# Performance work log

Hardware: AMD Instinct MI355X
Metric: run time of the kernel (lower is better)

The kernel has to match this reference:

```python
import jax, jax.numpy as jnp
import numpy as np

N, C, E, S = 16384, 128, 262144, 10
AVG_NUM_NEIGHBORS = 16.0
INV_SQRT3 = 1.0 / np.sqrt(3.0)


def setup_inputs() -> dict:
    key = jax.random.key(0)
    ks = jax.random.split(key, 15)
    return dict(
        node_specie=jax.random.randint(ks[0], (N,), 0, S),
        node_feats=jax.random.normal(ks[1], (N, C, 4), jnp.float32),   # irreps 0e+1o per channel
        edge_attrs=jax.random.normal(ks[2], (E, 4), jnp.float32),      # Y: 0e+1o
        edge_feats=jax.random.normal(ks[3], (E, 8), jnp.float32),      # radial scalars
        senders=jax.random.randint(ks[4], (E,), 0, N),
        receivers=jax.random.randint(ks[5], (E,), 0, N),
        W_sc0=jax.random.normal(ks[6], (S, C, C), jnp.float32),
        W_sc1=jax.random.normal(ks[7], (S, C, C), jnp.float32),
        W_pre0=jax.random.normal(ks[8], (C, C), jnp.float32),
        W_pre1=jax.random.normal(ks[9], (C, C), jnp.float32),
        W_mlp1=jax.random.normal(ks[10], (8, 64), jnp.float32),
        W_mlp2=jax.random.normal(ks[11], (64, 64), jnp.float32),
        W_mlp3=jax.random.normal(ks[12], (64, 4), jnp.float32),
        W_post0=jax.random.normal(ks[13], (C, 2, C), jnp.float32),
        W_post1=jax.random.normal(ks[14], (C, 2, C), jnp.float32),
    )


def reference(node_specie, node_feats, edge_attrs, edge_feats, senders, receivers,
              W_sc0, W_sc1, W_pre0, W_pre1, W_mlp1, W_mlp2, W_mlp3, W_post0, W_post1):
    inv_c = 1.0 / np.sqrt(C)
    s_in = node_feats[..., 0]      # [N,C] 0e
    v_in = node_feats[..., 1:4]    # [N,C,3] 1o

    # linear_sc: per-species equivariant linear (0e+1o -> hidden 0e+1o)
    sc_s = jnp.einsum('nc,ncd->nd', s_in, W_sc0[node_specie]) * inv_c
    sc_v = jnp.einsum('nci,ncd->ndi', v_in, W_sc1[node_specie]) * inv_c
    sc = jnp.concatenate([sc_s[..., None], sc_v], axis=-1)  # [N,C,4]

    # linear_premp: channel-mixing equivariant linear (same irreps)
    s = (s_in @ W_pre0) * inv_c                              # [N,C]
    v = jnp.einsum('nci,cd->ndi', v_in, W_pre1) * inv_c      # [N,C,3]

    # MessagePassingConvolution (channel axis kept instead of hk.vmap)
    se_s = s[senders]              # [E,C]
    se_v = v[senders]              # [E,C,3]
    a = edge_attrs[:, 1:4]         # drop 0e part of Y -> 1o
    dot = jnp.einsum('eci,ei->ec', se_v, a) * INV_SQRT3      # 1o x 1o -> 0e
    sva = se_s[..., None] * a[:, None, :]                    # 0e x 1o -> 1o

    # radial MLP -> one mixing scalar per irrep (num_irreps = 4), shared across channels
    h = jax.nn.silu((edge_feats @ W_mlp1) * (1.0 / np.sqrt(8.0)))
    h = jax.nn.silu((h @ W_mlp2) * 0.125)
    mix = (h @ W_mlp3) * 0.125                               # [E,4]

    # messages irreps 2x0e+2x1o: [s, dot | v, s*a], each block scaled by its mix scalar
    msg = jnp.concatenate([
        se_s[..., None] * mix[:, None, 0:1],
        dot[..., None] * mix[:, None, 1:2],
        se_v * mix[:, None, 2:3],
        sva * mix[:, None, 3:4],
    ], axis=-1)                                              # [E,C,8]

    agg = jnp.zeros((N, C, 8), msg.dtype).at[receivers].add(msg) / AVG_NUM_NEIGHBORS

    # linear_postmp: (2x0e+2x1o, C channels) -> (0e+1o, C channels)
    inv2c = 1.0 / np.sqrt(2 * C)
    o_s = jnp.einsum('ncm,cmd->nd', agg[..., :2], W_post0) * inv2c
    o_v = jnp.einsum('ncmi,cmd->ndi', agg[..., 2:].reshape(N, C, 2, 3), W_post1) * inv2c
    node_out = jnp.concatenate([o_s[..., None], o_v], axis=-1)  # [N,C,4]
    return node_out, sc
```

## Files before the change

### kernel.cpp

```cpp
#include <hip/hip_runtime.h>
#include <hip/hip_bf16.h>

#define N_NODES 16384
#define C_DIM   128
#define E_EDGES 262144
#define S_SPEC  10
#define CHUNK   256
#define PROWS   16544
#define PTILES  1034

__device__ __constant__ const float INV_C  = 0.08838834764831845f;
__device__ __constant__ const float INV_2C = 0.0625f;
#define F_INV_SQRT3 0.5773502691896258f
#define F_INV_SQRT8 0.35355339059327373f
#define F_INV_AVG   0.0625f

typedef __attribute__((ext_vector_type(8))) short bf16x8;
typedef __attribute__((ext_vector_type(4))) float f32x4;

__device__ __forceinline__ float silu(float x) {
    return x / (1.0f + __expf(-x));
}

__device__ __forceinline__ unsigned short f2bf(float x) {
    __hip_bfloat16 h = __float2bfloat16(x);
    return *reinterpret_cast<unsigned short*>(&h);
}

__device__ __forceinline__ unsigned int pack2bf(float lo, float hi) {
    return (unsigned int)f2bf(lo) | ((unsigned int)f2bf(hi) << 16);
}

__device__ __forceinline__ float bf2f(unsigned int u16) {
    return __uint_as_float((u16 & 0xffffu) << 16);
}

__device__ __forceinline__ float bf2f_hi(unsigned int u) {
    return __uint_as_float(u & 0xffff0000u);
}

__global__ __launch_bounds__(256) void init_kernel(
    int* __restrict__ counts, int* __restrict__ scnt,
    int* __restrict__ prow_map, int* __restrict__ tile_spec)
{
    const int idx = blockIdx.x * 256 + threadIdx.x;
    if (idx < N_NODES) counts[idx] = 0;
    if (idx < S_SPEC)  scnt[idx] = 0;
    if (idx < PROWS)   prow_map[idx] = -1;
    if (idx < PTILES)  tile_spec[idx] = 0;
}

__global__ __launch_bounds__(256) void hist_kernel(
    const int* __restrict__ receivers, int* __restrict__ cnt,
    const int* __restrict__ specie, int* __restrict__ scnt)
{
    __shared__ int h[S_SPEC];
    const int t = threadIdx.x;
    const bool doSpec = blockIdx.x < (N_NODES / 256);
    if (doSpec) {
        if (t < S_SPEC) h[t] = 0;
        __syncthreads();
        atomicAdd(&h[specie[blockIdx.x * 256 + t]], 1);
    }
    const int e = blockIdx.x * 256 + t;
    atomicAdd(&cnt[receivers[e]], 1);
    if (doSpec) {
        __syncthreads();
        if (t < S_SPEC) atomicAdd(&scnt[t], h[t]);
    }
}

__global__ __launch_bounds__(256) void scan_kernel(
    const int* __restrict__ cnt, int* __restrict__ start,
    int* __restrict__ cursor,
    const int* __restrict__ scnt, int* __restrict__ poff,
    int* __restrict__ scur)
{
    __shared__ int sums[256];
    const int t = threadIdx.x;
    if (t == 0) {
        int pa = 0;
        for (int i = 0; i < S_SPEC; ++i) {
            poff[i] = pa;
            scur[i] = 0;
            pa += ((scnt[i] + 15) >> 4) << 4;
        }
    }
    int s = 0;
    for (int i = 0; i < 64; ++i) s += cnt[t * 64 + i];
    sums[t] = s;
    __syncthreads();
    if (t == 0) {
        int a = 0;
        for (int i = 0; i < 256; ++i) { int v = sums[i]; sums[i] = a; a += v; }
    }
    __syncthreads();
    int a = sums[t];
    for (int i = 0; i < 64; ++i) {
        int v = cnt[t * 64 + i];
        start[t * 64 + i] = a;
        cursor[t * 64 + i] = a;
        a += v;
    }
    if (t == 255) start[N_NODES] = a;
}

__global__ __launch_bounds__(256) void scatter_place_kernel(
    const int* __restrict__ receivers, int* __restrict__ cursor,
    int* __restrict__ perm,
    const int* __restrict__ specie, const int* __restrict__ poff,
    int* __restrict__ scur,
    int* __restrict__ prow_map, int* __restrict__ tile_spec)
{
    const int t = threadIdx.x;
    const int e = blockIdx.x * 256 + t;
    const int pos = atomicAdd(&cursor[receivers[e]], 1);
    perm[pos] = e;

    if (blockIdx.x < (N_NODES / 256)) {
        __shared__ int h[S_SPEC];
        __shared__ int bbase[S_SPEC];
        if (t < S_SPEC) h[t] = 0;
        __syncthreads();
        const int n = blockIdx.x * 256 + t;
        const int s = specie[n];
        const int lrank = atomicAdd(&h[s], 1);
        __syncthreads();
        if (t < S_SPEC && h[t] > 0) bbase[t] = atomicAdd(&scur[t], h[t]);
        __syncthreads();
        const int p = poff[s] + bbase[s] + lrank;
        prow_map[p] = n;
        tile_spec[p >> 4] = s;
    }
}

__global__ __launch_bounds__(256) void prep_kernel(
    const int* __restrict__ prow_map, const float* __restrict__ node_feats,
    ushort* __restrict__ As, ushort* __restrict__ Av0,
    ushort* __restrict__ Av1, ushort* __restrict__ Av2,
    const float* __restrict__ Wsc0, const float* __restrict__ Wsc1,
    ushort* __restrict__ Wsc0t, ushort* __restrict__ Wsc1t,
    const float* __restrict__ Wpre0, const float* __restrict__ Wpre1,
    ushort* __restrict__ Wpre0t, ushort* __restrict__ Wpre1t,
    const float* __restrict__ Wp0, const float* __restrict__ Wp1,
    ushort* __restrict__ Bt0, ushort* __restrict__ Bt1,
    const float* __restrict__ Wm1, const float* __restrict__ Wm2,
    const float* __restrict__ Wm3,
    ushort* __restrict__ W1t, ushort* __restrict__ W2t,
    ushort* __restrict__ W3t)
{
    const int idx = blockIdx.x * 256 + threadIdx.x;
    {
        const int p = idx >> 7, c = idx & 127;
        const int nid = prow_map[p];
        float4 f = {0.0f, 0.0f, 0.0f, 0.0f};
        if (nid >= 0) f = ((const float4*)node_feats)[nid * C_DIM + c];
        As [idx] = f2bf(f.x);
        Av0[idx] = f2bf(f.y);
        Av1[idx] = f2bf(f.z);
        Av2[idx] = f2bf(f.w);
    }
    if (idx < S_SPEC * 128 * 128) {
        const int s = idx >> 14, d = (idx >> 7) & 127, k = idx & 127;
        Wsc0t[idx] = f2bf(Wsc0[s * 16384 + k * 128 + d] * INV_C);
        Wsc1t[idx] = f2bf(Wsc1[s * 16384 + k * 128 + d] * INV_C);
    }
    if (idx < 16384) {
        const int d = idx >> 7, k = idx & 127;
        Wpre0t[idx] = f2bf(Wpre0[k * 128 + d] * INV_C);
        Wpre1t[idx] = f2bf(Wpre1[k * 128 + d] * INV_C);
    }
    if (idx < 32768) {
        const int k = idx >> 7, d = idx & 127;
        Bt0[d * 256 + k] = f2bf(Wp0[idx] * INV_2C);
        Bt1[d * 256 + k] = f2bf(Wp1[idx] * INV_2C);
    }
    if (idx < 4096) {
        if (idx < 2048) {
            const int hh = idx >> 5, k = idx & 31;
            W1t[idx] = (k < 8) ? f2bf(Wm1[k * 64 + hh] * F_INV_SQRT8) : (ushort)0;
        }
        {
            const int c = idx >> 6, k = idx & 63;
            W2t[idx] = f2bf(Wm2[k * 64 + c] * 0.125f);
        }
        if (idx < 1024) {
            const int m = idx >> 6, k = idx & 63;
            W3t[idx] = (m < 4) ? f2bf(Wm3[k * 4 + m] * 0.125f) : (ushort)0;
        }
    }
}

__global__ __launch_bounds__(512) void node_gemm_kernel(
    const int* __restrict__ prow_map,
    const int* __restrict__ tile_spec,
    const ushort* __restrict__ As,
    const ushort* __restrict__ Av0,
    const ushort* __restrict__ Av1,
    const ushort* __restrict__ Av2,
    const ushort* __restrict__ Wsc0t,
    const ushort* __restrict__ Wsc1t,
    const ushort* __restrict__ Wpre0t,
    const ushort* __restrict__ Wpre1t,
    float* __restrict__ out_sc,
    ushort4* __restrict__ sv_bf)
{
    const int l  = threadIdx.x & 63;
    const int w  = threadIdx.x >> 6;
    const int d0 = w * 16;
    const int lr = l & 15;
    const int lg = l >> 4;

    bf16x8 bp0[4], bp1[4];
#pragma unroll
    for (int ks = 0; ks < 4; ++ks) {
        bp0[ks] = *reinterpret_cast<const bf16x8*>(
            Wpre0t + (d0 + lr) * 128 + ks * 32 + lg * 8);
        bp1[ks] = *reinterpret_cast<const bf16x8*>(
            Wpre1t + (d0 + lr) * 128 + ks * 32 + lg * 8);
    }

    const int tile = blockIdx.x;
    const int sp   = tile_spec[tile];
    const int r0   = tile * 16;

    const ushort* as  = As  + (size_t)(r0 + lr) * 128 + lg * 8;
    const ushort* av0 = Av0 + (size_t)(r0 + lr) * 128 + lg * 8;
    const ushort* av1 = Av1 + (size_t)(r0 + lr) * 128 + lg * 8;
    const ushort* av2 = Av2 + (size_t)(r0 + lr) * 128 + lg * 8;
    const ushort* ws0 = Wsc0t + (size_t)sp * 16384 + (d0 + lr) * 128 + lg * 8;
    const ushort* ws1 = Wsc1t + (size_t)sp * 16384 + (d0 + lr) * 128 + lg * 8;

    const f32x4 zero = {0.0f, 0.0f, 0.0f, 0.0f};
    f32x4 aS0 = zero, aS1 = zero, aS2 = zero, aS3 = zero;
    f32x4 aP0 = zero, aP1 = zero, aP2 = zero, aP3 = zero;

#pragma unroll
    for (int ks = 0; ks < 4; ++ks) {
        const bf16x8 a_s  = *reinterpret_cast<const bf16x8*>(as  + ks * 32);
        const bf16x8 a_v0 = *reinterpret_cast<const bf16x8*>(av0 + ks * 32);
        const bf16x8 a_v1 = *reinterpret_cast<const bf16x8*>(av1 + ks * 32);
        const bf16x8 a_v2 = *reinterpret_cast<const bf16x8*>(av2 + ks * 32);
        const bf16x8 bs0  = *reinterpret_cast<const bf16x8*>(ws0 + ks * 32);
        const bf16x8 bs1  = *reinterpret_cast<const bf16x8*>(ws1 + ks * 32);
        aS0 = __builtin_amdgcn_mfma_f32_16x16x32_bf16(a_s,  bs0, aS0, 0, 0, 0);
        aS1 = __builtin_amdgcn_mfma_f32_16x16x32_bf16(a_v0, bs1, aS1, 0, 0, 0);
        aS2 = __builtin_amdgcn_mfma_f32_16x16x32_bf16(a_v1, bs1, aS2, 0, 0, 0);
        aS3 = __builtin_amdgcn_mfma_f32_16x16x32_bf16(a_v2, bs1, aS3, 0, 0, 0);
        aP0 = __builtin_amdgcn_mfma_f32_16x16x32_bf16(a_s,  bp0[ks], aP0, 0, 0, 0);
        aP1 = __builtin_amdgcn_mfma_f32_16x16x32_bf16(a_v0, bp1[ks], aP1, 0, 0, 0);
        aP2 = __builtin_amdgcn_mfma_f32_16x16x32_bf16(a_v1, bp1[ks], aP2, 0, 0, 0);
        aP3 = __builtin_amdgcn_mfma_f32_16x16x32_bf16(a_v2, bp1[ks], aP3, 0, 0, 0);
    }

#pragma unroll
    for (int r = 0; r < 4; ++r) {
        const int row = r0 + lg * 4 + r;
        const int nid = prow_map[row];
        if (nid >= 0) {
            float4 o = {aS0[r], aS1[r], aS2[r], aS3[r]};
            ((float4*)out_sc)[(size_t)nid * C_DIM + (d0 + lr)] = o;
            ushort4 pv = {f2bf(aP0[r]), f2bf(aP1[r]), f2bf(aP2[r]), f2bf(aP3[r])};
            sv_bf[(size_t)nid * C_DIM + (d0 + lr)] = pv;
        }
    }
}

__global__ __launch_bounds__(256) void edge_mlp_mfma_kernel(
    const float* __restrict__ edge_feats,
    const float* __restrict__ edge_attrs,
    const ushort* __restrict__ W1t,
    const ushort* __restrict__ W2t,
    const ushort* __restrict__ W3t,
    uint4* __restrict__ coefbf)
{
    __shared__ ushort h_lds[4][16][72];

    const int w  = threadIdx.x >> 6;
    const int l  = threadIdx.x & 63;
    const int lr = l & 15;
    const int lg = l >> 4;

    bf16x8 a1[4];
#pragma unroll
    for (int mt = 0; mt < 4; ++mt)
        a1[mt] = *reinterpret_cast<const bf16x8*>(
            W1t + (mt * 16 + lr) * 32 + lg * 8);
    bf16x8 a2[4][2];
#pragma unroll
    for (int mt = 0; mt < 4; ++mt)
#pragma unroll
        for (int ks = 0; ks < 2; ++ks)
            a2[mt][ks] = *reinterpret_cast<const bf16x8*>(
                W2t + (mt * 16 + lr) * 64 + ks * 32 + lg * 8);
    bf16x8 a3[2];
#pragma unroll
    for (int ks = 0; ks < 2; ++ks)
        a3[ks] = *reinterpret_cast<const bf16x8*>(
            W3t + lr * 64 + ks * 32 + lg * 8);

    const int tile = blockIdx.x * 4 + w;
    const int e0   = tile * 16;
    const f32x4 zero = {0.0f, 0.0f, 0.0f, 0.0f};

    bf16x8 b1 = {0, 0, 0, 0, 0, 0, 0, 0};
    if (lg == 0) {
        const float4 q0 = *(const float4*)(edge_feats + (size_t)(e0 + lr) * 8);
        const float4 q1 = *(const float4*)(edge_feats + (size_t)(e0 + lr) * 8 + 4);
        b1[0] = (short)f2bf(q0.x); b1[1] = (short)f2bf(q0.y);
        b1[2] = (short)f2bf(q0.z); b1[3] = (short)f2bf(q0.w);
        b1[4] = (short)f2bf(q1.x); b1[5] = (short)f2bf(q1.y);
        b1[6] = (short)f2bf(q1.z); b1[7] = (short)f2bf(q1.w);
    }

    f32x4 d1[4];
#pragma unroll
    for (int mt = 0; mt < 4; ++mt)
        d1[mt] = __builtin_amdgcn_mfma_f32_16x16x32_bf16(a1[mt], b1, zero, 0, 0, 0);

#pragma unroll
    for (int mt = 0; mt < 4; ++mt) {
        uint2 p;
        p.x = pack2bf(silu(d1[mt][0]), silu(d1[mt][1]));
        p.y = pack2bf(silu(d1[mt][2]), silu(d1[mt][3]));
        *reinterpret_cast<uint2*>(&h_lds[w][lr][mt * 16 + lg * 4]) = p;
    }
    __syncthreads();

    bf16x8 b2[2];
#pragma unroll
    for (int ks = 0; ks < 2; ++ks)
        b2[ks] = *reinterpret_cast<const bf16x8*>(
            &h_lds[w][lr][ks * 32 + lg * 8]);

    f32x4 d2[4];
#pragma unroll
    for (int mt = 0; mt < 4; ++mt) {
        d2[mt] = __builtin_amdgcn_mfma_f32_16x16x32_bf16(a2[mt][0], b2[0], zero, 0, 0, 0);
        d2[mt] = __builtin_amdgcn_mfma_f32_16x16x32_bf16(a2[mt][1], b2[1], d2[mt], 0, 0, 0);
    }

#pragma unroll
    for (int mt = 0; mt < 4; ++mt) {
        uint2 p;
        p.x = pack2bf(silu(d2[mt][0]), silu(d2[mt][1]));
        p.y = pack2bf(silu(d2[mt][2]), silu(d2[mt][3]));
        *reinterpret_cast<uint2*>(&h_lds[w][lr][mt * 16 + lg * 4]) = p;
    }
    __syncthreads();

    bf16x8 b3[2];
#pragma unroll
    for (int ks = 0; ks < 2; ++ks)
        b3[ks] = *reinterpret_cast<const bf16x8*>(
            &h_lds[w][lr][ks * 32 + lg * 8]);

    f32x4 d3;
    d3 = __builtin_amdgcn_mfma_f32_16x16x32_bf16(a3[0], b3[0], zero, 0, 0, 0);
    d3 = __builtin_amdgcn_mfma_f32_16x16x32_bf16(a3[1], b3[1], d3, 0, 0, 0);

    if (lg == 0) {
        const int e = e0 + lr;
        const float4 a = *(const float4*)(edge_attrs + (size_t)e * 4);
        const float mx0 = d3[0], mx1 = d3[1], mx2 = d3[2], mx3 = d3[3];
        uint4 cv;
        cv.x = pack2bf(mx0,                      mx1 * a.y * F_INV_SQRT3);
        cv.y = pack2bf(mx1 * a.z * F_INV_SQRT3,  mx1 * a.w * F_INV_SQRT3);
        cv.z = pack2bf(mx2,                      mx3 * a.y);
        cv.w = pack2bf(mx3 * a.z,                mx3 * a.w);
        coefbf[e] = cv;
    }
}

__global__ __launch_bounds__(256) void agg_kernel(
    const int* __restrict__ start,
    const int* __restrict__ perm,
    const int* __restrict__ senders,
    const uint4* __restrict__ coefbf,
    const ushort4* __restrict__ sv_bf,
    unsigned int* __restrict__ A_s,
    unsigned int* __restrict__ A_v)
{
    __shared__ int   se_lds[CHUNK];
    __shared__ float sc_lds[CHUNK][8];

    const int n0   = blockIdx.x * 8;
    const int t    = threadIdx.x;
    const int c    = t & 127;
    const int half = t >> 7;

    int nbeg[4], nend[4];
#pragma unroll
    for (int k = 0; k < 4; ++k) {
        nbeg[k] = start[n0 + half * 4 + k];
        nend[k] = start[n0 + half * 4 + k + 1];
    }

    const int blk_beg = start[n0];
    const int blk_end = start[n0 + 8];

    float acc[4][8] = {};

    for (int cb = blk_beg; cb < blk_end; cb += CHUNK) {
        const int cn = min(CHUNK, blk_end - cb);
        __syncthreads();
        for (int j = t; j < cn; j += 256) {
            const int e = perm[cb + j];
            se_lds[j] = senders[e];
            const uint4 cv = coefbf[e];
            float4 lo = {bf2f(cv.x), bf2f_hi(cv.x), bf2f(cv.y), bf2f_hi(cv.y)};
            float4 hi = {bf2f(cv.z), bf2f_hi(cv.z), bf2f(cv.w), bf2f_hi(cv.w)};
            ((float4*)sc_lds[j])[0] = lo;
            ((float4*)sc_lds[j])[1] = hi;
        }
        __syncthreads();

#pragma unroll
        for (int k = 0; k < 4; ++k) {
            const int lo = max(nbeg[k], cb);
            const int hi = min(nend[k], cb + cn);
            int idx = lo;
            for (; idx + 2 <= hi; idx += 2) {
                const int j0 = idx - cb, j1 = j0 + 1;
                const int snd0 = se_lds[j0];
                const int snd1 = se_lds[j1];
                const ushort4 u0 = sv_bf[(size_t)snd0 * C_DIM + c];
                const ushort4 u1 = sv_bf[(size_t)snd1 * C_DIM + c];
                const float* kf0 = sc_lds[j0];
                const float* kf1 = sc_lds[j1];
                const float x0 = bf2f(u0.x), y0 = bf2f(u0.y),
                            z0 = bf2f(u0.z), w0 = bf2f(u0.w);
                const float x1 = bf2f(u1.x), y1 = bf2f(u1.y),
                            z1 = bf2f(u1.z), w1 = bf2f(u1.w);
                acc[k][0] += x0 * kf0[0];
                acc[k][1] += y0 * kf0[1] + z0 * kf0[2] + w0 * kf0[3];
                acc[k][2] += y0 * kf0[4];
                acc[k][3] += z0 * kf0[4];
                acc[k][4] += w0 * kf0[4];
                acc[k][5] += x0 * kf0[5];
                acc[k][6] += x0 * kf0[6];
                acc[k][7] += x0 * kf0[7];
                acc[k][0] += x1 * kf1[0];
                acc[k][1] += y1 * kf1[1] + z1 * kf1[2] + w1 * kf1[3];
                acc[k][2] += y1 * kf1[4];
                acc[k][3] += z1 * kf1[4];
                acc[k][4] += w1 * kf1[4];
                acc[k][5] += x1 * kf1[5];
                acc[k][6] += x1 * kf1[6];
                acc[k][7] += x1 * kf1[7];
            }
            if (idx < hi) {
                const int j = idx - cb;
                const int snd = se_lds[j];
                const ushort4 u = sv_bf[(size_t)snd * C_DIM + c];
                const float* kf = sc_lds[j];
                const float x = bf2f(u.x), y = bf2f(u.y),
                            z = bf2f(u.z), w = bf2f(u.w);
                acc[k][0] += x * kf[0];
                acc[k][1] += y * kf[1] + z * kf[2] + w * kf[3];
                acc[k][2] += y * kf[4];
                acc[k][3] += z * kf[4];
                acc[k][4] += w * kf[4];
                acc[k][5] += x * kf[5];
                acc[k][6] += x * kf[6];
                acc[k][7] += x * kf[7];
            }
        }
    }

#pragma unroll
    for (int k = 0; k < 4; ++k) {
        const int n = n0 + half * 4 + k;
        A_s[(size_t)n * 128 + c] =
            pack2bf(acc[k][0] * F_INV_AVG, acc[k][1] * F_INV_AVG);
        A_v[((size_t)0 * N_NODES + n) * 128 + c] =
            pack2bf(acc[k][2] * F_INV_AVG, acc[k][5] * F_INV_AVG);
        A_v[((size_t)1 * N_NODES + n) * 128 + c] =
            pack2bf(acc[k][3] * F_INV_AVG, acc[k][6] * F_INV_AVG);
        A_v[((size_t)2 * N_NODES + n) * 128 + c] =
            pack2bf(acc[k][4] * F_INV_AVG, acc[k][7] * F_INV_AVG);
    }
}

__global__ __launch_bounds__(512) void post_gemm_kernel(
    const ushort* __restrict__ A_s,
    const ushort* __restrict__ A_v,
    const ushort* __restrict__ Bt0,
    const ushort* __restrict__ Bt1,
    float4* __restrict__ out)
{
    const int l  = threadIdx.x & 63;
    const int w  = threadIdx.x >> 6;
    const int d0 = w * 16;
    const int lr = l & 15;
    const int lg = l >> 4;

    bf16x8 b0frag[8], b1frag[8];
#pragma unroll
    for (int ks = 0; ks < 8; ++ks) {
        b0frag[ks] = *reinterpret_cast<const bf16x8*>(
            Bt0 + (size_t)(d0 + lr) * 256 + ks * 32 + lg * 8);
        b1frag[ks] = *reinterpret_cast<const bf16x8*>(
            Bt1 + (size_t)(d0 + lr) * 256 + ks * 32 + lg * 8);
    }

    const int r0 = blockIdx.x * 16;
    const f32x4 zero = {0.0f, 0.0f, 0.0f, 0.0f};
    f32x4 accS = zero, acc0 = zero, acc1 = zero, acc2 = zero;

    const ushort* aS = A_s + (size_t)(r0 + lr) * 256 + lg * 8;
    const ushort* a0 = A_v + ((size_t)0 * N_NODES + r0 + lr) * 256 + lg * 8;
    const ushort* a1 = A_v + ((size_t)1 * N_NODES + r0 + lr) * 256 + lg * 8;
    const ushort* a2 = A_v + ((size_t)2 * N_NODES + r0 + lr) * 256 + lg * 8;

#pragma unroll
    for (int ks = 0; ks < 8; ++ks) {
        const bf16x8 fS = *reinterpret_cast<const bf16x8*>(aS + ks * 32);
        const bf16x8 f0 = *reinterpret_cast<const bf16x8*>(a0 + ks * 32);
        const bf16x8 f1 = *reinterpret_cast<const bf16x8*>(a1 + ks * 32);
        const bf16x8 f2 = *reinterpret_cast<const bf16x8*>(a2 + ks * 32);
        accS = __builtin_amdgcn_mfma_f32_16x16x32_bf16(fS, b0frag[ks], accS, 0, 0, 0);
        acc0 = __builtin_amdgcn_mfma_f32_16x16x32_bf16(f0, b1frag[ks], acc0, 0, 0, 0);
        acc1 = __builtin_amdgcn_mfma_f32_16x16x32_bf16(f1, b1frag[ks], acc1, 0, 0, 0);
        acc2 = __builtin_amdgcn_mfma_f32_16x16x32_bf16(f2, b1frag[ks], acc2, 0, 0, 0);
    }

#pragma unroll
    for (int r = 0; r < 4; ++r) {
        const int n = r0 + lg * 4 + r;
        float4 o = {accS[r], acc0[r], acc1[r], acc2[r]};
        out[(size_t)n * C_DIM + (d0 + lr)] = o;
    }
}

extern "C" void kernel_launch(void* const* d_in, const int* in_sizes, int n_in,
                              void* d_out, int out_size, void* d_ws, size_t ws_size,
                              hipStream_t stream)
{
    const int*   specie     = (const int*)d_in[0];
    const float* node_feats = (const float*)d_in[1];
    const float* edge_attrs = (const float*)d_in[2];
    const float* edge_feats = (const float*)d_in[3];
    const int*   senders    = (const int*)d_in[4];
    const int*   receivers  = (const int*)d_in[5];
    const float* Wsc0  = (const float*)d_in[6];
    const float* Wsc1  = (const float*)d_in[7];
    const float* Wpre0 = (const float*)d_in[8];
    const float* Wpre1 = (const float*)d_in[9];
    const float* Wm1   = (const float*)d_in[10];
    const float* Wm2   = (const float*)d_in[11];
    const float* Wm3   = (const float*)d_in[12];
    const float* Wp0   = (const float*)d_in[13];
    const float* Wp1   = (const float*)d_in[14];

    float* out_node = (float*)d_out;
    float* out_sc   = out_node + (size_t)N_NODES * C_DIM * 4;

    char* ws = (char*)d_ws;
    ushort4*      sv_bf = (ushort4*)ws;
    unsigned int* A_s   = (unsigned int*)(ws + (size_t)16 * 1024 * 1024);
    unsigned int* A_v   = A_s + (size_t)N_NODES * 128;
    uint4*        coefbf= (uint4*)(A_v + (size_t)3 * N_NODES * 128);
    ushort*       Asin  = (ushort*)(coefbf + (size_t)E_EDGES);
    ushort*       Av0in = Asin  + (size_t)PROWS * 128;
    ushort*       Av1in = Av0in + (size_t)PROWS * 128;
    ushort*       Av2in = Av1in + (size_t)PROWS * 128;
    ushort*       Bt0   = Av2in + (size_t)PROWS * 128;
    ushort*       Bt1   = Bt0 + 256 * 128;
    ushort*       Wsc0t = Bt1 + 256 * 128;
    ushort*       Wsc1t = Wsc0t + S_SPEC * 128 * 128;
    ushort*       Wpre0t = Wsc1t + S_SPEC * 128 * 128;
    ushort*       Wpre1t = Wpre0t + 128 * 128;
    ushort*       W1t   = Wpre1t + 128 * 128;
    ushort*       W2t   = W1t + 64 * 32;
    ushort*       W3t   = W2t + 64 * 64;
    int* counts    = (int*)(W3t + 16 * 64);
    int* start     = counts + N_NODES;
    int* cursor    = start + (N_NODES + 1);
    int* perm      = cursor + N_NODES;
    int* scnt      = perm + E_EDGES;
    int* poff      = scnt + S_SPEC;
    int* scur      = poff + S_SPEC;
    int* prow_map  = scur + S_SPEC;
    int* tile_spec = prow_map + PROWS;

    init_kernel<<<(PROWS + 255) / 256, 256, 0, stream>>>(
        counts, scnt, prow_map, tile_spec);

    hist_kernel<<<E_EDGES / 256, 256, 0, stream>>>(
        receivers, counts, specie, scnt);

    scan_kernel<<<1, 256, 0, stream>>>(counts, start, cursor, scnt, poff, scur);

    scatter_place_kernel<<<E_EDGES / 256, 256, 0, stream>>>(
        receivers, cursor, perm, specie, poff, scur, prow_map, tile_spec);

    prep_kernel<<<PROWS * 128 / 256, 256, 0, stream>>>(
        prow_map, node_feats, Asin, Av0in, Av1in, Av2in,
        Wsc0, Wsc1, Wsc0t, Wsc1t, Wpre0, Wpre1, Wpre0t, Wpre1t,
        Wp0, Wp1, Bt0, Bt1, Wm1, Wm2, Wm3, W1t, W2t, W3t);

    node_gemm_kernel<<<PTILES, 512, 0, stream>>>(
        prow_map, tile_spec, Asin, Av0in, Av1in, Av2in,
        Wsc0t, Wsc1t, Wpre0t, Wpre1t, out_sc, sv_bf);

    edge_mlp_mfma_kernel<<<E_EDGES / 64, 256, 0, stream>>>(
        edge_feats, edge_attrs, W1t, W2t, W3t, coefbf);

    agg_kernel<<<N_NODES / 8, 256, 0, stream>>>(
        start, perm, senders, coefbf, sv_bf, A_s, A_v);

    post_gemm_kernel<<<N_NODES / 16, 512, 0, stream>>>(
        (const ushort*)A_s, (const ushort*)A_v, Bt0, Bt1, (float4*)out_node);
}
```

Measured before the change: 228.2 us.

## Fuse post-message-passing linear GEMM into aggregation kernel via LDS staging

```diff
diff --git a/kernel.cpp b/kernel.cpp
--- a/kernel.cpp
+++ b/kernel.cpp
@@ -378,11 +378,13 @@
     const int* __restrict__ senders,
     const uint4* __restrict__ coefbf,
     const ushort4* __restrict__ sv_bf,
-    unsigned int* __restrict__ A_s,
-    unsigned int* __restrict__ A_v)
-{
-    __shared__ int   se_lds[CHUNK];
-    __shared__ float sc_lds[CHUNK][8];
+    const ushort* __restrict__ Bt0,
+    const ushort* __restrict__ Bt1,
+    float4* __restrict__ out)
+{
+    __shared__ int    se_lds[CHUNK];
+    __shared__ float  sc_lds[CHUNK][8];
+    __shared__ ushort a_lds[16][264];
 
     const int n0   = blockIdx.x * 8;
     const int t    = threadIdx.x;
@@ -468,68 +470,74 @@
         }
     }
 
+    unsigned int pv[4][4];
 #pragma unroll
     for (int k = 0; k < 4; ++k) {
-        const int n = n0 + half * 4 + k;
-        A_s[(size_t)n * 128 + c] =
-            pack2bf(acc[k][0] * F_INV_AVG, acc[k][1] * F_INV_AVG);
-        A_v[((size_t)0 * N_NODES + n) * 128 + c] =
-            pack2bf(acc[k][2] * F_INV_AVG, acc[k][5] * F_INV_AVG);
-        A_v[((size_t)1 * N_NODES + n) * 128 + c] =
-            pack2bf(acc[k][3] * F_INV_AVG, acc[k][6] * F_INV_AVG);
-        A_v[((size_t)2 * N_NODES + n) * 128 + c] =
-            pack2bf(acc[k][4] * F_INV_AVG, acc[k][7] * F_INV_AVG);
-    }
-}
-
-__global__ __launch_bounds__(512) void post_gemm_kernel(
-    const ushort* __restrict__ A_s,
-    const ushort* __restrict__ A_v,
-    const ushort* __restrict__ Bt0,
-    const ushort* __restrict__ Bt1,
-    float4* __restrict__ out)
-{
-    const int l  = threadIdx.x & 63;
-    const int w  = threadIdx.x >> 6;
-    const int d0 = w * 16;
+        pv[0][k] = pack2bf(acc[k][0] * F_INV_AVG, acc[k][1] * F_INV_AVG);
+        pv[1][k] = pack2bf(acc[k][2] * F_INV_AVG, acc[k][5] * F_INV_AVG);
+        pv[2][k] = pack2bf(acc[k][3] * F_INV_AVG, acc[k][6] * F_INV_AVG);
+        pv[3][k] = pack2bf(acc[k][4] * F_INV_AVG, acc[k][7] * F_INV_AVG);
+    }
+
+    const int l  = t & 63;
+    const int wv = t >> 6;
+    const int d0 = wv * 32;
     const int lr = l & 15;
     const int lg = l >> 4;
 
-    bf16x8 b0frag[8], b1frag[8];
-#pragma unroll
-    for (int ks = 0; ks < 8; ++ks) {
-        b0frag[ks] = *reinterpret_cast<const bf16x8*>(
-            Bt0 + (size_t)(d0 + lr) * 256 + ks * 32 + lg * 8);
-        b1frag[ks] = *reinterpret_cast<const bf16x8*>(
-            Bt1 + (size_t)(d0 + lr) * 256 + ks * 32 + lg * 8);
-    }
-
-    const int r0 = blockIdx.x * 16;
+    bf16x8 bt1f[2][8];
+#pragma unroll
+    for (int tt = 0; tt < 2; ++tt)
+#pragma unroll
+        for (int ks = 0; ks < 8; ++ks)
+            bt1f[tt][ks] = *reinterpret_cast<const bf16x8*>(
+                Bt1 + (size_t)(d0 + tt * 16 + lr) * 256 + ks * 32 + lg * 8);
+
     const f32x4 zero = {0.0f, 0.0f, 0.0f, 0.0f};
-    f32x4 accS = zero, acc0 = zero, acc1 = zero, acc2 = zero;
-
-    const ushort* aS = A_s + (size_t)(r0 + lr) * 256 + lg * 8;
-    const ushort* a0 = A_v + ((size_t)0 * N_NODES + r0 + lr) * 256 + lg * 8;
-    const ushort* a1 = A_v + ((size_t)1 * N_NODES + r0 + lr) * 256 + lg * 8;
-    const ushort* a2 = A_v + ((size_t)2 * N_NODES + r0 + lr) * 256 + lg * 8;
-
-#pragma unroll
-    for (int ks = 0; ks < 8; ++ks) {
-        const bf16x8 fS = *reinterpret_cast<const bf16x8*>(aS + ks * 32);
-        const bf16x8 f0 = *reinterpret_cast<const bf16x8*>(a0 + ks * 32);
-        const bf16x8 f1 = *reinterpret_cast<const bf16x8*>(a1 + ks * 32);
-        const bf16x8 f2 = *reinterpret_cast<const bf16x8*>(a2 + ks * 32);
-        accS = __builtin_amdgcn_mfma_f32_16x16x32_bf16(fS, b0frag[ks], accS, 0, 0, 0);
-        acc0 = __builtin_amdgcn_mfma_f32_16x16x32_bf16(f0, b1frag[ks], acc0, 0, 0, 0);
-        acc1 = __builtin_amdgcn_mfma_f32_16x16x32_bf16(f1, b1frag[ks], acc1, 0, 0, 0);
-        acc2 = __builtin_amdgcn_mfma_f32_16x16x32_bf16(f2, b1frag[ks], acc2, 0, 0, 0);
-    }
-
-#pragma unroll
-    for (int r = 0; r < 4; ++r) {
-        const int n = r0 + lg * 4 + r;
-        float4 o = {accS[r], acc0[r], acc1[r], acc2[r]};
-        out[(size_t)n * C_DIM + (d0 + lr)] = o;
+    f32x4 pS[2] = {zero, zero}, p0[2] = {zero, zero};
+    f32x4 p1[2] = {zero, zero}, p2[2] = {zero, zero};
+
+#pragma unroll
+    for (int p = 0; p < 4; ++p) {
+        __syncthreads();
+#pragma unroll
+        for (int k = 0; k < 4; ++k)
+            *reinterpret_cast<unsigned int*>(&a_lds[half * 4 + k][c * 2]) =
+                pv[p][k];
+        __syncthreads();
+#pragma unroll
+        for (int ks = 0; ks < 8; ++ks) {
+            const bf16x8 af = *reinterpret_cast<const bf16x8*>(
+                &a_lds[lr][ks * 32 + lg * 8]);
+#pragma unroll
+            for (int tt = 0; tt < 2; ++tt) {
+                bf16x8 bf;
+                if (p == 0)
+                    bf = *reinterpret_cast<const bf16x8*>(
+                        Bt0 + (size_t)(d0 + tt * 16 + lr) * 256 + ks * 32 + lg * 8);
+                else
+                    bf = bt1f[tt][ks];
+                if (p == 0)
+                    pS[tt] = __builtin_amdgcn_mfma_f32_16x16x32_bf16(af, bf, pS[tt], 0, 0, 0);
+                else if (p == 1)
+                    p0[tt] = __builtin_amdgcn_mfma_f32_16x16x32_bf16(af, bf, p0[tt], 0, 0, 0);
+                else if (p == 2)
+                    p1[tt] = __builtin_amdgcn_mfma_f32_16x16x32_bf16(af, bf, p1[tt], 0, 0, 0);
+                else
+                    p2[tt] = __builtin_amdgcn_mfma_f32_16x16x32_bf16(af, bf, p2[tt], 0, 0, 0);
+            }
+        }
+    }
+
+    if (lg < 2) {
+#pragma unroll
+        for (int tt = 0; tt < 2; ++tt)
+#pragma unroll
+            for (int r = 0; r < 4; ++r) {
+                const int n = n0 + lg * 4 + r;
+                float4 o = {pS[tt][r], p0[tt][r], p1[tt][r], p2[tt][r]};
+                out[(size_t)n * C_DIM + d0 + tt * 16 + lr] = o;
+            }
     }
 }
 
@@ -557,10 +565,8 @@
     float* out_sc   = out_node + (size_t)N_NODES * C_DIM * 4;
 
     char* ws = (char*)d_ws;
-    ushort4*      sv_bf = (ushort4*)ws;
-    unsigned int* A_s   = (unsigned int*)(ws + (size_t)16 * 1024 * 1024);
-    unsigned int* A_v   = A_s + (size_t)N_NODES * 128;
-    uint4*        coefbf= (uint4*)(A_v + (size_t)3 * N_NODES * 128);
+    ushort4*      sv_bf  = (ushort4*)ws;
+    uint4*        coefbf = (uint4*)(ws + (size_t)16 * 1024 * 1024);
     ushort*       Asin  = (ushort*)(coefbf + (size_t)E_EDGES);
     ushort*       Av0in = Asin  + (size_t)PROWS * 128;
     ushort*       Av1in = Av0in + (size_t)PROWS * 128;
@@ -608,8 +614,5 @@
         edge_feats, edge_attrs, W1t, W2t, W3t, coefbf);
 
     agg_kernel<<<N_NODES / 8, 256, 0, stream>>>(
-        start, perm, senders, coefbf, sv_bf, A_s, A_v);
-
-    post_gemm_kernel<<<N_NODES / 16, 512, 0, stream>>>(
-        (const ushort*)A_s, (const ushort*)A_v, Bt0, Bt1, (float4*)out_node);
-}
+        start, perm, senders, coefbf, sv_bf, Bt0, Bt1, (float4*)out_node);
+}
```

Measured after the change: 219.6 us (median of 2 runs). 1.04x faster.
